# Kernel tuning notes

Measured on AMD Instinct MI355X. Metric: run time of the kernel, lower is better.

Reference implementation:

```python
import jax, jax.numpy as jnp
import numpy as np

TEMP = 1.0
NUM_HEADS = 4


def tropical_linear(x, W, b, temperature=TEMP):
    # x: (..., in), W: (out, in), b: (out,)
    # y_i = T * logsumexp_j((W_ij + x_j)/T) + b_i  (soft tropical max-plus)
    z = W + x[..., None, :]                      # (..., out, in) broadcast tensor
    y = temperature * jax.nn.logsumexp(z / temperature, axis=-1)
    return y + b


def setup_inputs() -> dict:
    key = jax.random.key(0)
    ks = jax.random.split(key, 5)
    B, S, E = 32, 64, 256  # seq_len == head_dim (= E / num_heads) required by original code
    x = jax.random.normal(ks[0], (B, S, E), dtype=jnp.float32)
    mk = lambda k: 0.1 * jax.random.normal(k, (E, E), dtype=jnp.float32)
    zb = jnp.zeros((E,), dtype=jnp.float32)
    return {
        "x": x,
        "Wq": mk(ks[1]), "bq": zb,
        "Wk": mk(ks[2]), "bk": zb,
        "Wv": mk(ks[3]), "bv": zb,
        "Wo": mk(ks[4]), "bo": zb,
    }


def reference(x, Wq, bq, Wk, bk, Wv, bv, Wo, bo):
    B, S, E = x.shape
    H = NUM_HEADS
    D = E // H  # == S by construction (required by original matmul)

    q = tropical_linear(x, Wq, bq)  # (B,S,E)
    k = tropical_linear(x, Wk, bk)
    v = tropical_linear(x, Wv, bv)

    # (B,S,E) -> (B,H,S,D)
    split = lambda t: t.reshape(B, S, H, D).transpose(0, 2, 1, 3)
    q, k, v = split(q), split(k), split(v)

    # Original: (q.unsqueeze(-1) + k.unsqueeze(-2).transpose(-1,-2)).sum(-1)
    # Both operands are (B,H,S,D,1) -> scores == q + k elementwise, shape (B,H,S,D).
    scores = q + k
    attn = jax.nn.softmax(scores / TEMP, axis=-1)  # (B,H,S,D)

    # matmul (B,H,S,D) @ (B,H,S,D) valid since D == S
    out = jnp.einsum('bhsd,bhde->bhse', attn, v)   # (B,H,S,D)
    out = out.transpose(0, 2, 1, 3).reshape(B, S, E)
    return tropical_linear(out, Wo, bo)
```

## Files before the change

### kernel.cpp

```cpp
#include <hip/hip_runtime.h>

constexpr int ED = 256;
constexpr int SD = 64;
constexpr int BD = 32;
constexpr int NROWS = BD * SD;

typedef _Float16 half8 __attribute__((ext_vector_type(8)));
typedef float floatx4 __attribute__((ext_vector_type(4)));

__device__ inline unsigned short f2h(float f) {
  union { _Float16 h; unsigned short u; } c;
  c.h = (_Float16)f;
  return c.u;
}

__global__ __launch_bounds__(256) void expT_swz_kernel(
    const float* __restrict__ Wq, const float* __restrict__ Wk,
    const float* __restrict__ Wv, const float* __restrict__ Wo,
    unsigned short* __restrict__ EqS, unsigned short* __restrict__ EkS,
    unsigned short* __restrict__ EvS, unsigned short* __restrict__ EoS)
{
  int z = blockIdx.y;
  const float* W = (z == 0) ? Wq : (z == 1) ? Wk : (z == 2) ? Wv : Wo;
  unsigned short* out = (z == 0) ? EqS : (z == 1) ? EkS : (z == 2) ? EvS : EoS;
  int t = threadIdx.x;
  int n = blockIdx.x * 8 + (t >> 5), kl = t & 31;
#pragma unroll
  for (int kk = 0; kk < 8; ++kk)
    out[(kk * 256 + n) * 32 + kl] = f2h(__expf(W[n * ED + 32 * kk + kl]));
}

__global__ __launch_bounds__(256, 4) void qkv_mfma_kernel(
    const float* __restrict__ x,
    const unsigned short* __restrict__ EqS, const unsigned short* __restrict__ EkS,
    const unsigned short* __restrict__ EvS,
    const float* __restrict__ bq, const float* __restrict__ bk,
    const float* __restrict__ bv,
    unsigned short* __restrict__ AS, unsigned short* __restrict__ VS)
{
  int t = threadIdx.x;
  int w = t >> 6, lane = t & 63;
  int mt = blockIdx.x >> 2, h = blockIdx.x & 3;
  int row0 = mt * 16;

  __shared__ unsigned short aswz[8 * 512];
  __shared__ float fbuf[3][16][65];
  __shared__ float Mrow[16];

#pragma unroll
  for (int i = 0; i < 4; ++i) {
    int r = 4 * w + i;
    float4 xv = *(const float4*)&x[(size_t)(row0 + r) * ED + lane * 4];
    float m = fmaxf(fmaxf(xv.x, xv.y), fmaxf(xv.z, xv.w));
#pragma unroll
    for (int off = 32; off > 0; off >>= 1) m = fmaxf(m, __shfl_xor(m, off));
    ushort4 pk;
    pk.x = f2h(__expf(xv.x - m));
    pk.y = f2h(__expf(xv.y - m));
    pk.z = f2h(__expf(xv.z - m));
    pk.w = f2h(__expf(xv.w - m));
    int k0 = lane * 4;
    int idx = (k0 >> 5) * 512 + ((k0 >> 3) & 3) * 128 + r * 8 + (k0 & 7);
    *(ushort4*)&aswz[idx] = pk;
    if (lane == 0) Mrow[r] = m;
  }
  __syncthreads();

  half8 afrag[8];
#pragma unroll
  for (int kk = 0; kk < 8; ++kk)
    afrag[kk] = *(const half8*)&aswz[kk * 512 + lane * 8];

  int bb = ((h * 64 + w * 16 + (lane & 15)) << 2) + (lane >> 4);
  const half8* BQ = (const half8*)EqS;
  const half8* BK = (const half8*)EkS;
  const half8* BV = (const half8*)EvS;
  floatx4 accq = {0.f, 0.f, 0.f, 0.f};
  floatx4 acck = {0.f, 0.f, 0.f, 0.f};
  floatx4 accv = {0.f, 0.f, 0.f, 0.f};
#pragma unroll
  for (int kk = 0; kk < 8; ++kk) {
    half8 bqf = BQ[kk * 1024 + bb];
    half8 bkf = BK[kk * 1024 + bb];
    half8 bvf = BV[kk * 1024 + bb];
    accq = __builtin_amdgcn_mfma_f32_16x16x32_f16(afrag[kk], bqf, accq, 0, 0, 0);
    acck = __builtin_amdgcn_mfma_f32_16x16x32_f16(afrag[kk], bkf, acck, 0, 0, 0);
    accv = __builtin_amdgcn_mfma_f32_16x16x32_f16(afrag[kk], bvf, accv, 0, 0, 0);
  }

  {
    int c = w * 16 + (lane & 15);
    int rb = (lane >> 4) * 4;
#pragma unroll
    for (int reg = 0; reg < 4; ++reg) {
      fbuf[0][rb + reg][c] = accq[reg];
      fbuf[1][rb + reg][c] = acck[reg];
      fbuf[2][rb + reg][c] = accv[reg];
    }
  }
  __syncthreads();

  int cg = h * 64 + lane;
  float bqv = bq[cg], bkv = bk[cg], bvv = bv[cg];
  int b = row0 >> 6;
  int mt16 = (row0 >> 4) & 3;
  size_t asBase = (size_t)(((b * 4 + mt16) * 4) + h) * 1024
                + (lane >> 5) * 512 + ((lane >> 3) & 3) * 128 + (lane & 7);
#pragma unroll
  for (int i = 0; i < 4; ++i) {
    int r = 4 * w + i;
    float Mr = Mrow[r];
    float qv = Mr + __logf(fbuf[0][r][lane]) + bqv;
    float kv = Mr + __logf(fbuf[1][r][lane]) + bkv;
    float vv = Mr + __logf(fbuf[2][r][lane]) + bvv;
    int d = mt16 * 16 + r;
    VS[(size_t)(b * 2 + (d >> 5)) * 8192 + cg * 32 + ((d >> 3) & 3) * 8 + (d & 7)]
        = f2h(vv);
    float s = qv + kv;
    float sm = s;
#pragma unroll
    for (int off = 32; off > 0; off >>= 1) sm = fmaxf(sm, __shfl_xor(sm, off));
    float ex = __expf(s - sm);
    float den = ex;
#pragma unroll
    for (int off = 32; off > 0; off >>= 1) den += __shfl_xor(den, off);
    AS[asBase + r * 8] = f2h(ex / den);
  }
}

__global__ __launch_bounds__(256) void avo_mfma_kernel(
    const unsigned short* __restrict__ AS, const unsigned short* __restrict__ VS,
    const unsigned short* __restrict__ EoS, const float* __restrict__ bo,
    float* __restrict__ y)
{
  int t = threadIdx.x, w = t >> 6, lane = t & 63;
  int b = blockIdx.x >> 2, mt = blockIdx.x & 3;
  int row0 = b * 64 + mt * 16;
  int q = lane >> 4, nl = lane & 15;

  __shared__ float obuf[16][260];
  __shared__ unsigned short easwz[8 * 512];
  __shared__ float Mrow[16];

  const half8* AS8 = (const half8*)(AS + (size_t)(((b * 4 + mt) * 4) + w) * 1024);
  const half8* VS8 = (const half8*)VS;
  half8 af0 = AS8[lane], af1 = AS8[64 + lane];
  floatx4 acc[4];
#pragma unroll
  for (int nt = 0; nt < 4; ++nt) acc[nt] = (floatx4){0.f, 0.f, 0.f, 0.f};
#pragma unroll
  for (int nt = 0; nt < 4; ++nt) {
    int n = w * 64 + nt * 16 + nl;
    half8 b0 = VS8[(size_t)(b * 2 + 0) * 1024 + n * 4 + q];
    half8 b1 = VS8[(size_t)(b * 2 + 1) * 1024 + n * 4 + q];
    acc[nt] = __builtin_amdgcn_mfma_f32_16x16x32_f16(af0, b0, acc[nt], 0, 0, 0);
    acc[nt] = __builtin_amdgcn_mfma_f32_16x16x32_f16(af1, b1, acc[nt], 0, 0, 0);
  }
  int rb = q * 4;
#pragma unroll
  for (int nt = 0; nt < 4; ++nt)
#pragma unroll
    for (int reg = 0; reg < 4; ++reg)
      obuf[rb + reg][w * 64 + nt * 16 + nl] = acc[nt][reg];
  __syncthreads();

#pragma unroll
  for (int i = 0; i < 4; ++i) {
    int r = 4 * w + i;
    float4 o4 = *(const float4*)&obuf[r][lane * 4];
    float m = fmaxf(fmaxf(o4.x, o4.y), fmaxf(o4.z, o4.w));
#pragma unroll
    for (int off = 32; off > 0; off >>= 1) m = fmaxf(m, __shfl_xor(m, off));
    ushort4 pk;
    pk.x = f2h(__expf(o4.x - m));
    pk.y = f2h(__expf(o4.y - m));
    pk.z = f2h(__expf(o4.z - m));
    pk.w = f2h(__expf(o4.w - m));
    int k0 = lane * 4;
    int idx = (k0 >> 5) * 512 + ((k0 >> 3) & 3) * 128 + r * 8 + (k0 & 7);
    *(ushort4*)&easwz[idx] = pk;
    if (lane == 0) Mrow[r] = m;
  }
  __syncthreads();

  half8 af2[8];
#pragma unroll
  for (int kk = 0; kk < 8; ++kk)
    af2[kk] = *(const half8*)&easwz[kk * 512 + lane * 8];
  const half8* BO = (const half8*)EoS;
  floatx4 acc2[4];
#pragma unroll
  for (int nt = 0; nt < 4; ++nt) acc2[nt] = (floatx4){0.f, 0.f, 0.f, 0.f};
#pragma unroll
  for (int kk = 0; kk < 8; ++kk) {
#pragma unroll
    for (int nt = 0; nt < 4; ++nt) {
      int n = w * 64 + nt * 16 + nl;
      acc2[nt] = __builtin_amdgcn_mfma_f32_16x16x32_f16(
          af2[kk], BO[kk * 1024 + n * 4 + q], acc2[nt], 0, 0, 0);
    }
  }
#pragma unroll
  for (int nt = 0; nt < 4; ++nt)
#pragma unroll
    for (int reg = 0; reg < 4; ++reg)
      obuf[rb + reg][w * 64 + nt * 16 + nl] = acc2[nt][reg];
  __syncthreads();

  float4 bo4 = *(const float4*)&bo[lane * 4];
#pragma unroll
  for (int i = 0; i < 4; ++i) {
    int r = 4 * w + i;
    float4 f4 = *(const float4*)&obuf[r][lane * 4];
    float M = Mrow[r];
    float4 y4;
    y4.x = M + __logf(f4.x) + bo4.x;
    y4.y = M + __logf(f4.y) + bo4.y;
    y4.z = M + __logf(f4.z) + bo4.z;
    y4.w = M + __logf(f4.w) + bo4.w;
    *(float4*)&y[(size_t)(row0 + r) * ED + lane * 4] = y4;
  }
}

extern "C" void kernel_launch(void* const* d_in, const int* in_sizes, int n_in,
                              void* d_out, int out_size, void* d_ws, size_t ws_size,
                              hipStream_t stream) {
  const float* x  = (const float*)d_in[0];
  const float* Wq = (const float*)d_in[1];
  const float* bq = (const float*)d_in[2];
  const float* Wk = (const float*)d_in[3];
  const float* bk = (const float*)d_in[4];
  const float* Wv = (const float*)d_in[5];
  const float* bv = (const float*)d_in[6];
  const float* Wo = (const float*)d_in[7];
  const float* bo = (const float*)d_in[8];
  float* y = (float*)d_out;

  char* ws = (char*)d_ws;
  unsigned short* EqS = (unsigned short*)(ws);
  unsigned short* EkS = (unsigned short*)(ws + 131072);
  unsigned short* EvS = (unsigned short*)(ws + 262144);
  unsigned short* EoS = (unsigned short*)(ws + 393216);
  unsigned short* AS  = (unsigned short*)(ws + 524288);
  unsigned short* VS  = (unsigned short*)(ws + 524288 + 1048576);

  expT_swz_kernel<<<dim3(32, 4), 256, 0, stream>>>(Wq, Wk, Wv, Wo,
                                                   EqS, EkS, EvS, EoS);
  qkv_mfma_kernel<<<512, 256, 0, stream>>>(x, EqS, EkS, EvS, bq, bk, bv,
                                           AS, VS);
  avo_mfma_kernel<<<128, 256, 0, stream>>>(AS, VS, EoS, bo, y);
}
```

Measured before the change: 88.77 us.

## Prefetch QKV weight fragments early and split output projection across twice the blocks

In the QKV kernel, all x rows and every weight fragment for Q/K/V are loaded into registers up front, before the LDS staging and barrier. This hides global-memory latency behind the exp and shuffle work, at the cost of more registers, so the occupancy hint drops from 4 to 2. The AV/output kernel now launches 256 blocks instead of 128, each computing half of the output columns for the final tropical projection. That spreads the work over more CUs on a 256-CU part, but each block redoes the AV matmul and row exponentials.

```diff
diff --git a/kernel.cpp b/kernel.cpp
--- a/kernel.cpp
+++ b/kernel.cpp
@@ -30,7 +30,7 @@
     out[(kk * 256 + n) * 32 + kl] = f2h(__expf(W[n * ED + 32 * kk + kl]));
 }
 
-__global__ __launch_bounds__(256, 4) void qkv_mfma_kernel(
+__global__ __launch_bounds__(256, 2) void qkv_mfma_kernel(
     const float* __restrict__ x,
     const unsigned short* __restrict__ EqS, const unsigned short* __restrict__ EkS,
     const unsigned short* __restrict__ EvS,
@@ -47,18 +47,34 @@
   __shared__ float fbuf[3][16][65];
   __shared__ float Mrow[16];
 
-#pragma unroll
-  for (int i = 0; i < 4; ++i) {
-    int r = 4 * w + i;
-    float4 xv = *(const float4*)&x[(size_t)(row0 + r) * ED + lane * 4];
-    float m = fmaxf(fmaxf(xv.x, xv.y), fmaxf(xv.z, xv.w));
+  float4 xv[4];
+#pragma unroll
+  for (int i = 0; i < 4; ++i)
+    xv[i] = *(const float4*)&x[(size_t)(row0 + 4 * w + i) * ED + lane * 4];
+
+  int bb = ((h * 64 + w * 16 + (lane & 15)) << 2) + (lane >> 4);
+  const half8* BQ = (const half8*)EqS;
+  const half8* BK = (const half8*)EkS;
+  const half8* BV = (const half8*)EvS;
+  half8 bqf[8], bkf[8], bvf[8];
+#pragma unroll
+  for (int kk = 0; kk < 8; ++kk) {
+    bqf[kk] = BQ[kk * 1024 + bb];
+    bkf[kk] = BK[kk * 1024 + bb];
+    bvf[kk] = BV[kk * 1024 + bb];
+  }
+
+#pragma unroll
+  for (int i = 0; i < 4; ++i) {
+    int r = 4 * w + i;
+    float m = fmaxf(fmaxf(xv[i].x, xv[i].y), fmaxf(xv[i].z, xv[i].w));
 #pragma unroll
     for (int off = 32; off > 0; off >>= 1) m = fmaxf(m, __shfl_xor(m, off));
     ushort4 pk;
-    pk.x = f2h(__expf(xv.x - m));
-    pk.y = f2h(__expf(xv.y - m));
-    pk.z = f2h(__expf(xv.z - m));
-    pk.w = f2h(__expf(xv.w - m));
+    pk.x = f2h(__expf(xv[i].x - m));
+    pk.y = f2h(__expf(xv[i].y - m));
+    pk.z = f2h(__expf(xv[i].z - m));
+    pk.w = f2h(__expf(xv[i].w - m));
     int k0 = lane * 4;
     int idx = (k0 >> 5) * 512 + ((k0 >> 3) & 3) * 128 + r * 8 + (k0 & 7);
     *(ushort4*)&aswz[idx] = pk;
@@ -71,21 +87,14 @@
   for (int kk = 0; kk < 8; ++kk)
     afrag[kk] = *(const half8*)&aswz[kk * 512 + lane * 8];
 
-  int bb = ((h * 64 + w * 16 + (lane & 15)) << 2) + (lane >> 4);
-  const half8* BQ = (const half8*)EqS;
-  const half8* BK = (const half8*)EkS;
-  const half8* BV = (const half8*)EvS;
   floatx4 accq = {0.f, 0.f, 0.f, 0.f};
   floatx4 acck = {0.f, 0.f, 0.f, 0.f};
   floatx4 accv = {0.f, 0.f, 0.f, 0.f};
 #pragma unroll
   for (int kk = 0; kk < 8; ++kk) {
-    half8 bqf = BQ[kk * 1024 + bb];
-    half8 bkf = BK[kk * 1024 + bb];
-    half8 bvf = BV[kk * 1024 + bb];
-    accq = __builtin_amdgcn_mfma_f32_16x16x32_f16(afrag[kk], bqf, accq, 0, 0, 0);
-    acck = __builtin_amdgcn_mfma_f32_16x16x32_f16(afrag[kk], bkf, acck, 0, 0, 0);
-    accv = __builtin_amdgcn_mfma_f32_16x16x32_f16(afrag[kk], bvf, accv, 0, 0, 0);
+    accq = __builtin_amdgcn_mfma_f32_16x16x32_f16(afrag[kk], bqf[kk], accq, 0, 0, 0);
+    acck = __builtin_amdgcn_mfma_f32_16x16x32_f16(afrag[kk], bkf[kk], acck, 0, 0, 0);
+    accv = __builtin_amdgcn_mfma_f32_16x16x32_f16(afrag[kk], bvf[kk], accv, 0, 0, 0);
   }
 
   {
@@ -128,13 +137,14 @@
   }
 }
 
-__global__ __launch_bounds__(256) void avo_mfma_kernel(
+__global__ __launch_bounds__(256, 2) void avo_mfma_kernel(
     const unsigned short* __restrict__ AS, const unsigned short* __restrict__ VS,
     const unsigned short* __restrict__ EoS, const float* __restrict__ bo,
     float* __restrict__ y)
 {
   int t = threadIdx.x, w = t >> 6, lane = t & 63;
-  int b = blockIdx.x >> 2, mt = blockIdx.x & 3;
+  int blk = blockIdx.x;
+  int b = blk >> 3, mt = (blk >> 1) & 3, hf = blk & 1;
   int row0 = b * 64 + mt * 16;
   int q = lane >> 4, nl = lane & 15;
 
@@ -188,37 +198,36 @@
   for (int kk = 0; kk < 8; ++kk)
     af2[kk] = *(const half8*)&easwz[kk * 512 + lane * 8];
   const half8* BO = (const half8*)EoS;
-  floatx4 acc2[4];
-#pragma unroll
-  for (int nt = 0; nt < 4; ++nt) acc2[nt] = (floatx4){0.f, 0.f, 0.f, 0.f};
+  floatx4 acc2[2];
+  acc2[0] = (floatx4){0.f, 0.f, 0.f, 0.f};
+  acc2[1] = (floatx4){0.f, 0.f, 0.f, 0.f};
 #pragma unroll
   for (int kk = 0; kk < 8; ++kk) {
 #pragma unroll
-    for (int nt = 0; nt < 4; ++nt) {
-      int n = w * 64 + nt * 16 + nl;
+    for (int nt = 0; nt < 2; ++nt) {
+      int n = hf * 128 + w * 32 + nt * 16 + nl;
       acc2[nt] = __builtin_amdgcn_mfma_f32_16x16x32_f16(
           af2[kk], BO[kk * 1024 + n * 4 + q], acc2[nt], 0, 0, 0);
     }
   }
 #pragma unroll
-  for (int nt = 0; nt < 4; ++nt)
+  for (int nt = 0; nt < 2; ++nt)
 #pragma unroll
     for (int reg = 0; reg < 4; ++reg)
-      obuf[rb + reg][w * 64 + nt * 16 + nl] = acc2[nt][reg];
-  __syncthreads();
-
-  float4 bo4 = *(const float4*)&bo[lane * 4];
-#pragma unroll
-  for (int i = 0; i < 4; ++i) {
-    int r = 4 * w + i;
-    float4 f4 = *(const float4*)&obuf[r][lane * 4];
+      obuf[rb + reg][hf * 128 + w * 32 + nt * 16 + nl] = acc2[nt][reg];
+  __syncthreads();
+
+  int c0 = hf * 128 + lane * 2;
+  float2 bo2 = *(const float2*)&bo[c0];
+#pragma unroll
+  for (int i = 0; i < 4; ++i) {
+    int r = 4 * w + i;
+    float2 f2 = *(const float2*)&obuf[r][c0];
     float M = Mrow[r];
-    float4 y4;
-    y4.x = M + __logf(f4.x) + bo4.x;
-    y4.y = M + __logf(f4.y) + bo4.y;
-    y4.z = M + __logf(f4.z) + bo4.z;
-    y4.w = M + __logf(f4.w) + bo4.w;
-    *(float4*)&y[(size_t)(row0 + r) * ED + lane * 4] = y4;
+    float2 y2;
+    y2.x = M + __logf(f2.x) + bo2.x;
+    y2.y = M + __logf(f2.y) + bo2.y;
+    *(float2*)&y[(size_t)(row0 + r) * ED + c0] = y2;
   }
 }
 
@@ -248,5 +257,5 @@
                                                    EqS, EkS, EvS, EoS);
   qkv_mfma_kernel<<<512, 256, 0, stream>>>(x, EqS, EkS, EvS, bq, bk, bv,
                                            AS, VS);
-  avo_mfma_kernel<<<128, 256, 0, stream>>>(AS, VS, EoS, bo, y);
-}
+  avo_mfma_kernel<<<256, 256, 0, stream>>>(AS, VS, EoS, bo, y);
+}
```

Measured after the change: 86.69 us. 2.3% less time.
